# Optimization experiments

Measured on AMD Instinct MI355X. Metric: run time of the kernel, lower is better.

The kernel has to match this reference:

```python
import jax, jax.numpy as jnp
import numpy as np

B, S, D, H = 2, 2048, 1024, 16
HD = D // H  # head_features = 64
MASKED_BIAS = -10000.0


def setup_inputs() -> dict:
    key = jax.random.key(0)
    ks = jax.random.split(key, 5)
    return {
        "hidden_states": jax.random.normal(ks[0], (B, S, D), dtype=jnp.float32),
        "c_attn_w": jax.random.normal(ks[1], (D, 3 * D), dtype=jnp.float32) * 0.02,
        "c_attn_b": jax.random.normal(ks[2], (3 * D,), dtype=jnp.float32) * 0.02,
        "c_proj_w": jax.random.normal(ks[3], (D, D), dtype=jnp.float32) * 0.02,
        "c_proj_b": jax.random.normal(ks[4], (D,), dtype=jnp.float32) * 0.02,
    }


def reference(hidden_states, c_attn_w, c_attn_b, c_proj_w, c_proj_b):
    b, s, d = hidden_states.shape
    # Conv1D: x @ W + b, projecting D -> 3D, then split into q, k, v
    qkv = hidden_states @ c_attn_w + c_attn_b  # [b, s, 3D]
    q, k, v = jnp.split(qkv, 3, axis=-1)
    # split heads -> [b, H, s, HD]
    q = q.reshape(b, s, H, HD).transpose(0, 2, 1, 3)
    k = k.reshape(b, s, H, HD).transpose(0, 2, 1, 3)
    v = v.reshape(b, s, H, HD).transpose(0, 2, 1, 3)
    # scaled scores: [b, H, s, s]
    w = jnp.einsum("bhqd,bhkd->bhqk", q, k) / jnp.sqrt(jnp.float32(HD))
    # causal mask (tril bias buffer) applied via where with masked_bias
    causal = jnp.tril(jnp.ones((s, s), dtype=bool))
    w = jnp.where(causal[None, None], w, jnp.float32(MASKED_BIAS))
    p = jax.nn.softmax(w, axis=-1)  # attn_dropout p=0
    a = jnp.einsum("bhqk,bhkd->bhqd", p, v)  # [b, H, s, HD]
    # merge heads -> [b, s, D], output projection (resid_dropout p=0)
    a = a.transpose(0, 2, 1, 3).reshape(b, s, d)
    return a @ c_proj_w + c_proj_b
```

## Files before the change

kernel.cpp:

```cpp
#include <hip/hip_runtime.h>

typedef unsigned short u16;
typedef unsigned int   u32;

typedef __attribute__((ext_vector_type(8))) short bf16x8;
typedef __attribute__((ext_vector_type(4))) short bf16x4;
typedef __attribute__((ext_vector_type(4))) float f32x4;

typedef const __attribute__((address_space(1))) u32 gq_t;
typedef __attribute__((address_space(3))) u32 lq_t;

__device__ __forceinline__ float b2f(u16 u) {
    union { u32 u; float f; } c; c.u = ((u32)u) << 16; return c.f;
}
__device__ __forceinline__ u16 f2b(float f) {
    union { float f; u32 u; } c; c.f = f;
    u32 r = c.u + 0x7fffu + ((c.u >> 16) & 1u);
    return (u16)(r >> 16);
}
__device__ __forceinline__ u16 f2b_hu(float f) {
    union { float f; u32 u; } c; c.f = f;
    return (u16)((c.u + 0x8000u) >> 16);
}

__global__ __launch_bounds__(256) void convert_x(const float* __restrict__ in,
                                                 u16* __restrict__ out) {
    const int i = (blockIdx.x * 256 + threadIdx.x) * 8;
    f32x4 a = *(const f32x4*)(in + i);
    f32x4 b = *(const f32x4*)(in + i + 4);
    union { bf16x8 v; u16 u[8]; } o;
    o.u[0] = f2b(a[0]); o.u[1] = f2b(a[1]); o.u[2] = f2b(a[2]); o.u[3] = f2b(a[3]);
    o.u[4] = f2b(b[0]); o.u[5] = f2b(b[1]); o.u[6] = f2b(b[2]); o.u[7] = f2b(b[3]);
    *(bf16x8*)(out + i) = o.v;
}

__global__ __launch_bounds__(256) void transpose_w(const float* __restrict__ in,
                                                   u16* __restrict__ out, int N) {
    __shared__ float t[32][33];
    const int k0 = blockIdx.y * 32, n0 = blockIdx.x * 32;
    const int tid = threadIdx.x;
    const int kr = tid >> 3, nc = (tid & 7) * 4;
    f32x4 v = *(const f32x4*)(in + (size_t)(k0 + kr) * N + n0 + nc);
    t[kr][nc] = v[0]; t[kr][nc + 1] = v[1]; t[kr][nc + 2] = v[2]; t[kr][nc + 3] = v[3];
    __syncthreads();
    const int nr = tid >> 3, kc = (tid & 7) * 4;
    union { bf16x4 v; u16 a[4]; } o;
    o.a[0] = f2b(t[kc][nr]);     o.a[1] = f2b(t[kc + 1][nr]);
    o.a[2] = f2b(t[kc + 2][nr]); o.a[3] = f2b(t[kc + 3][nr]);
    *(bf16x4*)(out + (size_t)(n0 + nr) * 1024 + k0 + kc) = o.v;
}

__global__ __launch_bounds__(256) void gemm128(
    const u16* __restrict__ A, const u16* __restrict__ WT,
    const float* __restrict__ bias, float* __restrict__ out,
    u16* __restrict__ Qb, u16* __restrict__ Kb, u16* __restrict__ Vt,
    int N, int K, int mode)
{
    __shared__ u16 As[128 * 32];
    __shared__ u16 Bs[128 * 32];
    const int tid  = threadIdx.x;
    const int m0   = blockIdx.y * 128, n0 = blockIdx.x * 128;
    const int wv   = tid >> 6, lane = tid & 63;
    const int wm   = (wv >> 1) * 64, wn = (wv & 1) * 64;
    const int l16  = lane & 15, quad = lane >> 4;

    const int sr = lane >> 2, sc = (lane & 3) * 8;
    const int rbase = wv * 16 + sr;

    f32x4 acc[4][4];
    const f32x4 zero = {0.f, 0.f, 0.f, 0.f};
    #pragma unroll
    for (int i = 0; i < 4; i++)
        #pragma unroll
        for (int j = 0; j < 4; j++) acc[i][j] = zero;

    for (int k0 = 0; k0 < K; k0 += 32) {
        #pragma unroll
        for (int c = 0; c < 2; c++) {
            const int rl = c * 64 + rbase;
            const u16* ag = A  + (size_t)(m0 + rl) * K + k0 + sc;
            const u16* bg = WT + (size_t)(n0 + rl) * K + k0 + sc;
            __builtin_amdgcn_global_load_lds((gq_t*)ag, (lq_t*)&As[(c * 64 + wv * 16) * 32], 16, 0, 0);
            __builtin_amdgcn_global_load_lds((gq_t*)bg, (lq_t*)&Bs[(c * 64 + wv * 16) * 32], 16, 0, 0);
        }
        __syncthreads();
        bf16x8 af[4], bf[4];
        #pragma unroll
        for (int i = 0; i < 4; i++) {
            af[i] = *(const bf16x8*)&As[(wm + i * 16 + l16) * 32 + quad * 8];
            bf[i] = *(const bf16x8*)&Bs[(wn + i * 16 + l16) * 32 + quad * 8];
        }
        #pragma unroll
        for (int i = 0; i < 4; i++)
            #pragma unroll
            for (int j = 0; j < 4; j++)
                acc[i][j] = __builtin_amdgcn_mfma_f32_16x16x32_bf16(af[i], bf[j], acc[i][j], 0, 0, 0);
        __syncthreads();
    }

    #pragma unroll
    for (int j = 0; j < 4; j++) {
        const int nn = n0 + wn + j * 16 + l16;
        const float bvf = bias[nn];
        #pragma unroll
        for (int i = 0; i < 4; i++) {
            float o[4];
            #pragma unroll
            for (int r = 0; r < 4; r++) o[r] = acc[i][j][r] + bvf;
            const int mbase = m0 + wm + i * 16 + quad * 4;
            if (mode == 0) {
                #pragma unroll
                for (int r = 0; r < 4; r++)
                    out[(size_t)(mbase + r) * N + nn] = o[r];
            } else {
                const int part = nn >> 10, w = nn & 1023;
                const int h = w >> 6, d = w & 63;
                const int b = mbase >> 11, s = mbase & 2047;
                const size_t bh = (size_t)b * 16 + h;
                if (part == 2) {
                    union { bf16x4 v; u16 a[4]; } pk;
                    #pragma unroll
                    for (int r = 0; r < 4; r++) pk.a[r] = f2b(o[r]);
                    *(bf16x4*)(Vt + (bh * 64 + d) * 2048 + s) = pk.v;
                } else {
                    u16* t = (part == 0) ? Qb : Kb;
                    const float scl = (part == 0) ? 0.125f : 1.0f;
                    #pragma unroll
                    for (int r = 0; r < 4; r++)
                        t[(bh * 2048 + s + r) * 64 + d] = f2b(o[r] * scl);
                }
            }
        }
    }
}

__global__ __launch_bounds__(256, 3) void attn_mfma(
    const u16* __restrict__ Qb, const u16* __restrict__ Kb,
    const u16* __restrict__ Vt, u16* __restrict__ Aout)
{
    const int bx   = blockIdx.x;
    const int x    = bx & 511, half = bx >> 9;
    const int xcd  = x & 7, y = x >> 3;
    const int bh   = xcd * 4 + (y & 3);
    const int pidx = y >> 2;
    const int chunk = half ? (31 - pidx) : pidx;
    const int q0   = chunk * 64;

    const int tid  = threadIdx.x;
    const int wave = tid >> 6, lane = tid & 63;
    const int l16  = lane & 15, quad = lane >> 4;
    const int qw   = q0 + wave * 16;
    const size_t kbase = (size_t)bh * 2048 * 64;
    const size_t vbase = (size_t)bh * 64 * 2048;

    __shared__ __align__(16) u16 Ks[2][64 * 72];
    __shared__ __align__(16) u16 Vs[2][64 * 72];
    __shared__ __align__(16) u16 p_all[4][16 * 72];
    u16* p_lds = p_all[wave];

    const u16* qp = Qb + kbase + (size_t)(qw + l16) * 64 + quad * 8;
    bf16x8 aq0 = *(const bf16x8*)qp;
    bf16x8 aq1 = *(const bf16x8*)(qp + 32);

    union { bf16x8 v; u16 a[8]; } onesu;
    #pragma unroll
    for (int j = 0; j < 8; j++) onesu.a[j] = 0x3F80;
    const bf16x8 vones = onesu.v;

    f32x4 oacc[4], lacc;
    const f32x4 zero = {0.f, 0.f, 0.f, 0.f};
    #pragma unroll
    for (int t = 0; t < 4; t++) oacc[t] = zero;
    lacc = zero;

    const int srow = tid >> 2, scol = (tid & 3) * 16;
    u16* ksw0 = &Ks[0][srow * 72 + scol];
    u16* vsw0 = &Vs[0][srow * 72 + scol];
    u16* ksw1 = &Ks[1][srow * 72 + scol];
    u16* vsw1 = &Vs[1][srow * 72 + scol];

    {
        const u16* kg = Kb + kbase + (size_t)srow * 64 + scol;
        const u16* vg = Vt + vbase + (size_t)srow * 2048 + scol;
        bf16x8 k0 = *(const bf16x8*)kg, k1 = *(const bf16x8*)(kg + 8);
        bf16x8 v0 = *(const bf16x8*)vg, v1 = *(const bf16x8*)(vg + 8);
        *(bf16x8*)ksw0 = k0; *(bf16x8*)(ksw0 + 8) = k1;
        *(bf16x8*)vsw0 = v0; *(bf16x8*)(vsw0 + 8) = v1;
    }
    __syncthreads();

    for (int kt = 0; kt <= chunk; kt++) {
        const int kb = kt * 64, buf = kt & 1;

        bf16x8 pk0, pk1, pv0, pv1;
        const bool pf = (kt < chunk);
        if (pf) {
            const u16* kg = Kb + kbase + (size_t)(kb + 64 + srow) * 64 + scol;
            const u16* vg = Vt + vbase + (size_t)srow * 2048 + (kb + 64) + scol;
            pk0 = *(const bf16x8*)kg; pk1 = *(const bf16x8*)(kg + 8);
            pv0 = *(const bf16x8*)vg; pv1 = *(const bf16x8*)(vg + 8);
        }

        const u16* Kl = Ks[buf];
        const u16* Vl = Vs[buf];
        bf16x8 kk[8], vv[8];
        #pragma unroll
        for (int t = 0; t < 4; t++) {
            #pragma unroll
            for (int ks = 0; ks < 2; ks++) {
                kk[2 * t + ks] = *(const bf16x8*)&Kl[(16 * t + l16) * 72 + ks * 32 + quad * 8];
                vv[2 * t + ks] = *(const bf16x8*)&Vl[(16 * t + l16) * 72 + ks * 32 + quad * 8];
            }
        }

        f32x4 sc[4];
        #pragma unroll
        for (int t = 0; t < 4; t++) {
            sc[t] = __builtin_amdgcn_mfma_f32_16x16x32_bf16(aq0, kk[2 * t],     zero,  0, 0, 0);
            sc[t] = __builtin_amdgcn_mfma_f32_16x16x32_bf16(aq1, kk[2 * t + 1], sc[t], 0, 0, 0);
        }

        const bool diag = (kt == chunk);
        #pragma unroll
        for (int r = 0; r < 4; r++) {
            const int qi = qw + quad * 4 + r;
            u16* pw = &p_lds[(quad * 4 + r) * 72 + l16];
            #pragma unroll
            for (int t = 0; t < 4; t++) {
                float pv = __expf(sc[t][r]);
                if (diag && (kb + 16 * t + l16 > qi)) pv = 0.f;
                pw[16 * t] = f2b_hu(pv);
            }
        }

        __asm__ volatile("s_waitcnt lgkmcnt(0)");

        #pragma unroll
        for (int ks = 0; ks < 2; ks++) {
            bf16x8 ap = *(const bf16x8*)&p_lds[l16 * 72 + ks * 32 + quad * 8];
            #pragma unroll
            for (int t = 0; t < 4; t++)
                oacc[t] = __builtin_amdgcn_mfma_f32_16x16x32_bf16(ap, vv[2 * t + ks], oacc[t], 0, 0, 0);
            lacc = __builtin_amdgcn_mfma_f32_16x16x32_bf16(ap, vones, lacc, 0, 0, 0);
        }

        if (pf) {
            if (buf) { *(bf16x8*)ksw0 = pk0; *(bf16x8*)(ksw0 + 8) = pk1;
                       *(bf16x8*)vsw0 = pv0; *(bf16x8*)(vsw0 + 8) = pv1; }
            else     { *(bf16x8*)ksw1 = pk0; *(bf16x8*)(ksw1 + 8) = pk1;
                       *(bf16x8*)vsw1 = pv0; *(bf16x8*)(vsw1 + 8) = pv1; }
        }
        __syncthreads();
    }

    const int b = bh >> 4, h = bh & 15;
    #pragma unroll
    for (int r = 0; r < 4; r++) {
        const float inv = 1.0f / lacc[r];
        const int qi = qw + quad * 4 + r;
        u16* dst = Aout + (size_t)(b * 2048 + qi) * 1024 + h * 64 + l16;
        #pragma unroll
        for (int t = 0; t < 4; t++)
            dst[16 * t] = f2b(oacc[t][r] * inv);
    }
}

extern "C" void kernel_launch(void* const* d_in, const int* in_sizes, int n_in,
                              void* d_out, int out_size, void* d_ws, size_t ws_size,
                              hipStream_t stream)
{
    const float* X    = (const float*)d_in[0];
    const float* Wqkv = (const float*)d_in[1];
    const float* Bqkv = (const float*)d_in[2];
    const float* Wp   = (const float*)d_in[3];
    const float* Bp   = (const float*)d_in[4];
    float* out = (float*)d_out;

    char* ws = (char*)d_ws;
    u16* WqkvT = (u16*)(ws);
    u16* WprojT= (u16*)(ws + 6291456);
    u16* Qb    = (u16*)(ws + 8388608);
    u16* Kb    = (u16*)(ws + 16777216);
    u16* Vt    = (u16*)(ws + 25165824);
    u16* Ab    = (u16*)(ws + 33554432);
    u16* Xb    = (u16*)(ws + 41943040);

    convert_x<<<dim3(2048), 256, 0, stream>>>(X, Xb);
    transpose_w<<<dim3(96, 32), 256, 0, stream>>>(Wqkv, WqkvT, 3072);
    transpose_w<<<dim3(32, 32), 256, 0, stream>>>(Wp, WprojT, 1024);

    gemm128<<<dim3(24, 32), 256, 0, stream>>>(Xb, WqkvT, Bqkv, nullptr,
                                              Qb, Kb, Vt, 3072, 1024, 1);
    attn_mfma<<<dim3(1024), 256, 0, stream>>>(Qb, Kb, Vt, Ab);
    gemm128<<<dim3(8, 32), 256, 0, stream>>>(Ab, WprojT, Bp, out,
                                             nullptr, nullptr, nullptr, 1024, 1024, 0);
}
```

Before: 187.8 us.

## Fuse prep kernels, swizzle GEMM LDS, add narrower-tile output projection GEMM

Merges the X conversion and both weight transposes into a single prep launch to cut launch overhead. Adds an XOR swizzle to the GEMM LDS layout, applied on both the global_load_lds store side and the fragment read side, to reduce bank conflicts. Replaces the output projection with a 128x64-tile GEMM that launches twice as many blocks (512 instead of 256) to fill more CUs. The narrower tile lowers data reuse per block.

```diff
diff --git a/kernel.cpp b/kernel.cpp
--- a/kernel.cpp
+++ b/kernel.cpp
@@ -23,22 +23,27 @@
     return (u16)((c.u + 0x8000u) >> 16);
 }
 
-__global__ __launch_bounds__(256) void convert_x(const float* __restrict__ in,
-                                                 u16* __restrict__ out) {
-    const int i = (blockIdx.x * 256 + threadIdx.x) * 8;
-    f32x4 a = *(const f32x4*)(in + i);
-    f32x4 b = *(const f32x4*)(in + i + 4);
-    union { bf16x8 v; u16 u[8]; } o;
-    o.u[0] = f2b(a[0]); o.u[1] = f2b(a[1]); o.u[2] = f2b(a[2]); o.u[3] = f2b(a[3]);
-    o.u[4] = f2b(b[0]); o.u[5] = f2b(b[1]); o.u[6] = f2b(b[2]); o.u[7] = f2b(b[3]);
-    *(bf16x8*)(out + i) = o.v;
-}
-
-__global__ __launch_bounds__(256) void transpose_w(const float* __restrict__ in,
-                                                   u16* __restrict__ out, int N) {
+__global__ __launch_bounds__(256) void prep(
+    const float* __restrict__ X,    u16* __restrict__ Xb,
+    const float* __restrict__ Wqkv, u16* __restrict__ WqkvT,
+    const float* __restrict__ Wp,   u16* __restrict__ WprojT)
+{
     __shared__ float t[32][33];
-    const int k0 = blockIdx.y * 32, n0 = blockIdx.x * 32;
-    const int tid = threadIdx.x;
+    const int bid = blockIdx.x, tid = threadIdx.x;
+    if (bid < 2048) {
+        const int i = (bid * 256 + tid) * 8;
+        f32x4 a = *(const f32x4*)(X + i);
+        f32x4 b = *(const f32x4*)(X + i + 4);
+        union { bf16x8 v; u16 u[8]; } o;
+        o.u[0] = f2b(a[0]); o.u[1] = f2b(a[1]); o.u[2] = f2b(a[2]); o.u[3] = f2b(a[3]);
+        o.u[4] = f2b(b[0]); o.u[5] = f2b(b[1]); o.u[6] = f2b(b[2]); o.u[7] = f2b(b[3]);
+        *(bf16x8*)(Xb + i) = o.v;
+        return;
+    }
+    const float* in; u16* out; int N, bx, by;
+    if (bid < 5120) { const int b2 = bid - 2048; in = Wqkv; out = WqkvT; N = 3072; bx = b2 % 96; by = b2 / 96; }
+    else            { const int b3 = bid - 5120; in = Wp;   out = WprojT; N = 1024; bx = b3 & 31; by = b3 >> 5; }
+    const int k0 = by * 32, n0 = bx * 32;
     const int kr = tid >> 3, nc = (tid & 7) * 4;
     f32x4 v = *(const f32x4*)(in + (size_t)(k0 + kr) * N + n0 + nc);
     t[kr][nc] = v[0]; t[kr][nc + 1] = v[1]; t[kr][nc + 2] = v[2]; t[kr][nc + 3] = v[3];
@@ -50,6 +55,7 @@
     *(bf16x4*)(out + (size_t)(n0 + nr) * 1024 + k0 + kc) = o.v;
 }
 
+
 __global__ __launch_bounds__(256) void gemm128(
     const u16* __restrict__ A, const u16* __restrict__ WT,
     const float* __restrict__ bias, float* __restrict__ out,
@@ -64,8 +70,10 @@
     const int wm   = (wv >> 1) * 64, wn = (wv & 1) * 64;
     const int l16  = lane & 15, quad = lane >> 4;
 
-    const int sr = lane >> 2, sc = (lane & 3) * 8;
+    const int sr = lane >> 2;
+    const int sc = (((lane & 3) ^ ((lane >> 3) & 3)) * 8);
     const int rbase = wv * 16 + sr;
+    const int rsw = ((l16 >> 1) & 3) * 8;
 
     f32x4 acc[4][4];
     const f32x4 zero = {0.f, 0.f, 0.f, 0.f};
@@ -87,8 +95,8 @@
         bf16x8 af[4], bf[4];
         #pragma unroll
         for (int i = 0; i < 4; i++) {
-            af[i] = *(const bf16x8*)&As[(wm + i * 16 + l16) * 32 + quad * 8];
-            bf[i] = *(const bf16x8*)&Bs[(wn + i * 16 + l16) * 32 + quad * 8];
+            af[i] = *(const bf16x8*)&As[(wm + i * 16 + l16) * 32 + ((quad * 8) ^ rsw)];
+            bf[i] = *(const bf16x8*)&Bs[(wn + i * 16 + l16) * 32 + ((quad * 8) ^ rsw)];
         }
         #pragma unroll
         for (int i = 0; i < 4; i++)
@@ -134,6 +142,66 @@
     }
 }
 
+__global__ __launch_bounds__(256) void gemm_proj(
+    const u16* __restrict__ A, const u16* __restrict__ WT,
+    const float* __restrict__ bias, float* __restrict__ out, int N, int K)
+{
+    __shared__ u16 As[128 * 32];
+    __shared__ u16 Bs[64 * 32];
+    const int tid  = threadIdx.x;
+    const int m0   = blockIdx.y * 128, n0 = blockIdx.x * 64;
+    const int wv   = tid >> 6, lane = tid & 63;
+    const int wm   = (wv >> 1) * 64, wn = (wv & 1) * 32;
+    const int l16  = lane & 15, quad = lane >> 4;
+
+    const int sr = lane >> 2;
+    const int sc = (((lane & 3) ^ ((lane >> 3) & 3)) * 8);
+    const int rbase = wv * 16 + sr;
+    const int rsw = ((l16 >> 1) & 3) * 8;
+
+    f32x4 acc[4][2];
+    const f32x4 zero = {0.f, 0.f, 0.f, 0.f};
+    #pragma unroll
+    for (int i = 0; i < 4; i++) { acc[i][0] = zero; acc[i][1] = zero; }
+
+    for (int k0 = 0; k0 < K; k0 += 32) {
+        #pragma unroll
+        for (int c = 0; c < 2; c++) {
+            const u16* ag = A + (size_t)(m0 + c * 64 + rbase) * K + k0 + sc;
+            __builtin_amdgcn_global_load_lds((gq_t*)ag, (lq_t*)&As[(c * 64 + wv * 16) * 32], 16, 0, 0);
+        }
+        const u16* bg = WT + (size_t)(n0 + rbase) * K + k0 + sc;
+        __builtin_amdgcn_global_load_lds((gq_t*)bg, (lq_t*)&Bs[(wv * 16) * 32], 16, 0, 0);
+        __syncthreads();
+        bf16x8 af[4], bf[2];
+        #pragma unroll
+        for (int i = 0; i < 4; i++)
+            af[i] = *(const bf16x8*)&As[(wm + i * 16 + l16) * 32 + ((quad * 8) ^ rsw)];
+        #pragma unroll
+        for (int j = 0; j < 2; j++)
+            bf[j] = *(const bf16x8*)&Bs[(wn + j * 16 + l16) * 32 + ((quad * 8) ^ rsw)];
+        #pragma unroll
+        for (int i = 0; i < 4; i++)
+            #pragma unroll
+            for (int j = 0; j < 2; j++)
+                acc[i][j] = __builtin_amdgcn_mfma_f32_16x16x32_bf16(af[i], bf[j], acc[i][j], 0, 0, 0);
+        __syncthreads();
+    }
+
+    #pragma unroll
+    for (int j = 0; j < 2; j++) {
+        const int nn = n0 + wn + j * 16 + l16;
+        const float bvf = bias[nn];
+        #pragma unroll
+        for (int i = 0; i < 4; i++) {
+            const int mbase = m0 + wm + i * 16 + quad * 4;
+            #pragma unroll
+            for (int r = 0; r < 4; r++)
+                out[(size_t)(mbase + r) * N + nn] = acc[i][j][r] + bvf;
+        }
+    }
+}
+
 __global__ __launch_bounds__(256, 3) void attn_mfma(
     const u16* __restrict__ Qb, const u16* __restrict__ Kb,
     const u16* __restrict__ Vt, u16* __restrict__ Aout)
@@ -285,13 +353,10 @@
     u16* Ab    = (u16*)(ws + 33554432);
     u16* Xb    = (u16*)(ws + 41943040);
 
-    convert_x<<<dim3(2048), 256, 0, stream>>>(X, Xb);
-    transpose_w<<<dim3(96, 32), 256, 0, stream>>>(Wqkv, WqkvT, 3072);
-    transpose_w<<<dim3(32, 32), 256, 0, stream>>>(Wp, WprojT, 1024);
+    prep<<<dim3(6144), 256, 0, stream>>>(X, Xb, Wqkv, WqkvT, Wp, WprojT);
 
     gemm128<<<dim3(24, 32), 256, 0, stream>>>(Xb, WqkvT, Bqkv, nullptr,
                                               Qb, Kb, Vt, 3072, 1024, 1);
     attn_mfma<<<dim3(1024), 256, 0, stream>>>(Qb, Kb, Vt, Ab);
-    gemm128<<<dim3(8, 32), 256, 0, stream>>>(Ab, WprojT, Bp, out,
-                                             nullptr, nullptr, nullptr, 1024, 1024, 0);
-}
+    gemm_proj<<<dim3(16, 32), 256, 0, stream>>>(Ab, WprojT, Bp, out, 1024, 1024);
+}
```

Result: faster. 178.4 us (-5.0%).
